# Kernel optimization log

Measured on AMD Instinct MI355X. Metric: run time of the kernel, lower is better.

The kernel has to match this reference:

```python
import math
import jax, jax.numpy as jnp
import numpy as np
from jax import lax

B, S, T = 16, 1200, 600
D, V, FF = 1024, 1404, 2048
H, DH, PERIOD, WID = 4, 256, 25, 8


def setup_inputs() -> dict:
    key = jax.random.key(0)
    ks = jax.random.split(key, 24)
    w = lambda i, shape: jax.random.normal(ks[i], shape, dtype=jnp.float32) * 0.02
    return {
        "audio_embedding": jax.random.normal(ks[0], (B, S, 768), dtype=jnp.float32),
        "vertice": jax.random.normal(ks[1], (B, T, 3, 468), dtype=jnp.float32),
        "W_af": w(2, (D, 768)), "b_af": w(3, (D,)),
        "sa_Wq": w(4, (D, D)), "sa_bq": w(5, (D,)),
        "sa_Wk": w(6, (D, D)), "sa_bk": w(7, (D,)),
        "sa_Wv": w(8, (D, D)), "sa_bv": w(9, (D,)),
        "sa_Wo": w(10, (D, D)), "sa_bo": w(11, (D,)),
        "ca_Wq": w(12, (D, D)), "ca_bq": w(13, (D,)),
        "ca_Wk": w(14, (D, D)), "ca_bk": w(15, (D,)),
        "ca_Wv": w(16, (D, D)), "ca_bv": w(17, (D,)),
        "ca_Wo": w(18, (D, D)), "ca_bo": w(19, (D,)),
        "ln1_g": jnp.ones((D,), jnp.float32), "ln1_b": jnp.zeros((D,), jnp.float32),
        "ln2_g": jnp.ones((D,), jnp.float32), "ln2_b": jnp.zeros((D,), jnp.float32),
        "ln3_g": jnp.ones((D,), jnp.float32), "ln3_b": jnp.zeros((D,), jnp.float32),
        "W_ff1": w(20, (FF, D)), "b_ff1": jnp.zeros((FF,), jnp.float32),
        "W_ff2": w(21, (D, FF)), "b_ff2": jnp.zeros((D,), jnp.float32),
        "W_vm": w(22, (D, V)), "b_vm": jnp.zeros((D,), jnp.float32),
        "W_vr": w(23, (V, D)), "b_vr": jnp.zeros((V,), jnp.float32),
    }


def _pe_table():
    # PeriodicPositionalEncoding: sin/cos table of length `period`, tiled over time
    pos = np.arange(PERIOD, dtype=np.float32)[:, None]
    div = np.exp(np.arange(0, D, 2, dtype=np.float32) * (-math.log(10000.0) / D))
    pe = np.zeros((PERIOD, D), dtype=np.float32)
    pe[:, 0::2] = np.sin(pos * div)
    pe[:, 1::2] = np.cos(pos * div)
    return jnp.asarray(pe)


def _slopes():
    start = 2.0 ** (-2.0 ** (-(math.log2(H) - 3.0)))
    return jnp.asarray(start * start ** np.arange(H, dtype=np.float32), dtype=jnp.float32)


def _ln(x, g, b):
    m = jnp.mean(x, -1, keepdims=True)
    v = jnp.mean((x - m) ** 2, -1, keepdims=True)
    return (x - m) / jnp.sqrt(v + 1e-5) * g + b


def reference(audio_embedding, vertice, W_af, b_af, sa_Wq, sa_bq, sa_Wk, sa_bk, sa_Wv, sa_bv, sa_Wo, sa_bo, ca_Wq, ca_bq, ca_Wk, ca_bk, ca_Wv, ca_bv, ca_Wo, ca_bo, ln1_g, ln1_b, ln2_g, ln2_b, ln3_g, ln3_b, W_ff1, b_ff1, W_ff2, b_ff2, W_vm, b_vm, W_vr, b_vr):
    # The torch loop reruns the full causal decoder on the growing prefix each frame;
    # because the tgt mask is strictly causal (ALiBi bias depends only on i-j), the
    # math is exactly equivalent to an incremental decode with a self-attn KV cache.
    pe, slopes = _pe_table(), _slopes()
    scale = 1.0 / math.sqrt(DH)
    NEG = -1e9
    hidden = audio_embedding @ W_af.T + b_af              # (B,S,D) audio_feature_map
    mem_k = (hidden @ ca_Wk.T + ca_bk).reshape(B, S, H, DH)
    mem_v = (hidden @ ca_Wv.T + ca_bv).reshape(B, S, H, DH)
    t_idx = jnp.arange(T)
    s_idx = jnp.arange(S)
    emb0 = jnp.broadcast_to(b_vm, (B, D))                 # vertice_map(zeros)
    kc0 = jnp.zeros((T, B, D), jnp.float32)
    vc0 = jnp.zeros((T, B, D), jnp.float32)

    def step(carry, i):
        emb, kc, vc = carry
        x = emb + pe[i % PERIOD]                          # PPE (B,D)
        q = (x @ sa_Wq.T + sa_bq).reshape(B, H, DH)
        kc = kc.at[i].set(x @ sa_Wk.T + sa_bk)
        vc = vc.at[i].set(x @ sa_Wv.T + sa_bv)
        kh = kc.reshape(T, B, H, DH)
        vh = vc.reshape(T, B, H, DH)
        rel = i - t_idx                                   # ALiBi: alibi[i,j] = -floor((i-j)/period)
        bias = slopes[:, None] * (-(jnp.maximum(rel, 0) // PERIOD)).astype(jnp.float32)
        sc = jnp.einsum('bhd,tbhd->bht', q, kh) * scale + bias[None]
        sc = jnp.where((t_idx <= i)[None, None, :], sc, NEG)
        sa = jnp.einsum('bht,tbhd->bhd', jax.nn.softmax(sc, -1), vh).reshape(B, D)
        x = _ln(x + sa @ sa_Wo.T + sa_bo, ln1_g, ln1_b)
        q2 = (x @ ca_Wq.T + ca_bq).reshape(B, H, DH)
        sc2 = jnp.einsum('bhd,bshd->bhs', q2, mem_k) * scale
        allowed = (s_idx >= 2 * i - (WID - 2)) & (s_idx < 2 * i + 2)   # enc_dec_mask window
        sc2 = jnp.where(allowed[None, None, :], sc2, NEG)
        ca = jnp.einsum('bhs,bshd->bhd', jax.nn.softmax(sc2, -1), mem_v).reshape(B, D)
        x = _ln(x + ca @ ca_Wo.T + ca_bo, ln2_g, ln2_b)
        ff = jax.nn.relu(x @ W_ff1.T + b_ff1) @ W_ff2.T + b_ff2
        x = _ln(x + ff, ln3_g, ln3_b)
        out_v = x @ W_vr.T + b_vr                         # vertice_map_r (B,V)
        emb_next = out_v @ W_vm.T + b_vm                  # vertice_map of last output
        return (emb_next, kc, vc), out_v

    _, outs = lax.scan(step, (emb0, kc0, vc0), t_idx)
    vertice_out = jnp.transpose(outs, (1, 0, 2))          # (B,T,V)
    loss = jnp.mean((vertice_out - vertice.reshape(B, T, -1)) ** 2)
    return loss
```

## Files before the change

### kernel.cpp

```cpp
#include <hip/hip_runtime.h>

typedef unsigned short u16;
typedef short s16x8 __attribute__((ext_vector_type(8)));
typedef float f32x4 __attribute__((ext_vector_type(4)));
typedef float f32x2 __attribute__((ext_vector_type(2)));
typedef unsigned u32x2 __attribute__((ext_vector_type(2)));

#define DEV static __device__ __forceinline__

DEV float bf2f(u16 h){ union{unsigned u;float f;} v; v.u=((unsigned)h)<<16; return v.f; }
DEV u16 f2bf(float f){ union{float f;unsigned u;} v; v.f=f; unsigned u=v.u; return (u16)((u + 0x7fffu + ((u>>16)&1u))>>16); }

DEV void st2_dc(u16* p, u16 v){
  unsigned vv = v;
  asm volatile("global_store_short %0, %1, off sc0 sc1" :: "v"(p), "v"(vv) : "memory");
}
DEV void st16_dc(void* p, s16x8 v){
  asm volatile("global_store_dwordx4 %0, %1, off sc0 sc1" :: "v"(p), "v"(v) : "memory");
}
DEV void stf_dc(float* p, float v){
  asm volatile("global_store_dword %0, %1, off sc0 sc1" :: "v"(p), "v"(v) : "memory");
}
DEV u16 ld2_dc(const u16* p){
  unsigned r;
  asm volatile("global_load_ushort %0, %1, off sc0 sc1\n\ts_waitcnt vmcnt(0)" : "=&v"(r) : "v"(p) : "memory");
  return (u16)r;
}
DEV void vmwait0(){ asm volatile("s_waitcnt vmcnt(0)" ::: "memory"); }

DEV void ldf8_dc(const u16* p, s16x8* o){
  asm volatile(
    "global_load_dwordx4 %0, %8, off sc0 sc1\n\t"
    "global_load_dwordx4 %1, %8, off offset:64 sc0 sc1\n\t"
    "global_load_dwordx4 %2, %8, off offset:128 sc0 sc1\n\t"
    "global_load_dwordx4 %3, %8, off offset:192 sc0 sc1\n\t"
    "global_load_dwordx4 %4, %8, off offset:256 sc0 sc1\n\t"
    "global_load_dwordx4 %5, %8, off offset:320 sc0 sc1\n\t"
    "global_load_dwordx4 %6, %8, off offset:384 sc0 sc1\n\t"
    "global_load_dwordx4 %7, %8, off offset:448 sc0 sc1\n\t"
    "s_waitcnt vmcnt(0)"
    : "=&v"(o[0]),"=&v"(o[1]),"=&v"(o[2]),"=&v"(o[3]),
// ... 3 lines not shown
DEV void ldf8r_dc(const u16* p, s16x8* o, const u16* pr, unsigned* rr){
  asm volatile(
    "global_load_dwordx4 %0, %9, off sc0 sc1\n\t"
    "global_load_dwordx4 %1, %9, off offset:64 sc0 sc1\n\t"
    "global_load_dwordx4 %2, %9, off offset:128 sc0 sc1\n\t"
    "global_load_dwordx4 %3, %9, off offset:192 sc0 sc1\n\t"
    "global_load_dwordx4 %4, %9, off offset:256 sc0 sc1\n\t"
    "global_load_dwordx4 %5, %9, off offset:320 sc0 sc1\n\t"
    "global_load_dwordx4 %6, %9, off offset:384 sc0 sc1\n\t"
    "global_load_dwordx4 %7, %9, off offset:448 sc0 sc1\n\t"
    "global_load_ushort %8, %10, off sc0 sc1\n\t"
    "s_waitcnt vmcnt(0)"
    : "=&v"(o[0]),"=&v"(o[1]),"=&v"(o[2]),"=&v"(o[3]),
      "=&v"(o[4]),"=&v"(o[5]),"=&v"(o[6]),"=&v"(o[7]),"=&v"(*rr)
    : "v"(p), "v"(pr) : "memory");
}
DEV void ldf8rs_dc(const u16* p, s16x8* o, const u16* pr, unsigned* rr, const float* ps, f32x2* ss){
  asm volatile(
    "global_load_dwordx4 %0, %10, off sc0 sc1\n\t"
    "global_load_dwordx4 %1, %10, off offset:64 sc0 sc1\n\t"
    "global_load_dwordx4 %2, %10, off offset:128 sc0 sc1\n\t"
    "global_load_dwordx4 %3, %10, off offset:192 sc0 sc1\n\t"
    "global_load_dwordx4 %4, %10, off offset:256 sc0 sc1\n\t"
    "global_load_dwordx4 %5, %10, off offset:320 sc0 sc1\n\t"
    "global_load_dwordx4 %6, %10, off offset:384 sc0 sc1\n\t"
    "global_load_dwordx4 %7, %10, off offset:448 sc0 sc1\n\t"
    "global_load_ushort %8, %11, off sc0 sc1\n\t"
    "global_load_dwordx2 %9, %12, off sc0 sc1\n\t"
    "s_waitcnt vmcnt(0)"
    : "=&v"(o[0]),"=&v"(o[1]),"=&v"(o[2]),"=&v"(o[3]),
      "=&v"(o[4]),"=&v"(o[5]),"=&v"(o[6]),"=&v"(o[7]),"=&v"(*rr),"=&v"(*ss)
    : "v"(p), "v"(pr), "v"(ps) : "memory");
}
DEV void ldf16rs_dc(const u16* p, s16x8* o, const u16* pr, unsigned* rr, const float* ps, f32x2* ss){
  asm volatile(
    "global_load_dwordx4 %0, %18, off sc0 sc1\n\t"
    "global_load_dwordx4 %1, %18, off offset:64 sc0 sc1\n\t"
    "global_load_dwordx4 %2, %18, off offset:128 sc0 sc1\n\t"
    "global_load_dwordx4 %3, %18, off offset:192 sc0 sc1\n\t"
    "global_load_dwordx4 %4, %18, off offset:256 sc0 sc1\n\t"
    "global_load_dwordx4 %5, %18, off offset:320 sc0 sc1\n\t"
    "global_load_dwordx4 %6, %18, off offset:384 sc0 sc1\n\t"
    "global_load_dwordx4 %7, %18, off offset:448 sc0 sc1\n\t"
    "global_load_dwordx4 %8, %18, off offset:2048 sc0 sc1\n\t"
    "global_load_dwordx4 %9, %18, off offset:2112 sc0 sc1\n\t"
    "global_load_dwordx4 %10, %18, off offset:2176 sc0 sc1\n\t"
    "global_load_dwordx4 %11, %18, off offset:2240 sc0 sc1\n\t"
// ... 4 lines not shown
    "global_load_ushort %16, %19, off sc0 sc1\n\t"
    "global_load_dwordx2 %17, %20, off sc0 sc1\n\t"
    "s_waitcnt vmcnt(0)"
    : "=&v"(o[0]),"=&v"(o[1]),"=&v"(o[2]),"=&v"(o[3]),
      "=&v"(o[4]),"=&v"(o[5]),"=&v"(o[6]),"=&v"(o[7]),
      "=&v"(o[8]),"=&v"(o[9]),"=&v"(o[10]),"=&v"(o[11]),
      "=&v"(o[12]),"=&v"(o[13]),"=&v"(o[14]),"=&v"(o[15]),
      "=&v"(*rr),"=&v"(*ss)
    : "v"(p), "v"(pr), "v"(ps) : "memory");
}

constexpr size_t SZ_DD = (size_t)1024*1024*2;
constexpr size_t OFF_WQ2=0;
constexpr size_t OFF_WK2=OFF_WQ2+SZ_DD;
constexpr size_t OFF_WV2=OFF_WK2+SZ_DD;
constexpr size_t OFF_WO=OFF_WV2+SZ_DD;
constexpr size_t OFF_CAWQ=OFF_WO+SZ_DD;
constexpr size_t OFF_CAWO=OFF_CAWQ+SZ_DD;
constexpr size_t OFF_FF1=OFF_CAWO+SZ_DD;
constexpr size_t OFF_FF2=OFF_FF1+(size_t)2048*1024*2;
constexpr size_t OFF_MB =OFF_FF2+(size_t)2048*1024*2;
constexpr size_t OFF_WVR=OFF_MB+SZ_DD;
constexpr size_t OFF_WKP=OFF_WVR+(size_t)1404*1024*2;
constexpr size_t OFF_WVP=OFF_WKP+(size_t)1024*768*2;
constexpr size_t OFF_WAFT=OFF_WVP+(size_t)1024*768*2;
constexpr size_t OFF_WVRT=OFF_WAFT+(size_t)768*1024*2;
constexpr size_t OFF_PE  =OFF_WVRT+(size_t)1024*1408*2;
constexpr size_t OFF_BKP =OFF_PE+25*1024*4;
constexpr size_t OFF_BVP =OFF_BKP+4096;
constexpr size_t OFF_BCOMB=OFF_BVP+4096;
constexpr size_t OFF_MEMK=OFF_BCOMB+4096;
constexpr size_t OFF_MEMV=OFF_MEMK+(size_t)16*1200*1024*2;
constexpr size_t OFF_KC  =OFF_MEMV+(size_t)16*1200*1024*2;
constexpr size_t OFF_VC  =OFF_KC+(size_t)600*16*1024*2;
constexpr size_t OFF_U3S =OFF_VC+(size_t)600*16*1024*2;
constexpr size_t OFF_ST3 =OFF_U3S+(size_t)600*16*1024*2;
constexpr size_t OFF_XB  =OFF_ST3+600*32*4;
constexpr size_t OFF_QB  =OFF_XB+32768;
constexpr size_t OFF_SC  =OFF_QB+32768;
constexpr size_t OFF_SA  =OFF_SC+(size_t)16*4*608*4;
constexpr size_t OFF_U1  =OFF_SA+32768;
constexpr size_t OFF_ST1 =OFF_U1+32768;
constexpr size_t OFF_Q2  =OFF_ST1+256;
constexpr size_t OFF_CA  =OFF_Q2+32768;
constexpr size_t OFF_U2  =OFF_CA+32768;
constexpr size_t OFF_ST2 =OFF_U2+32768;
constexpr size_t OFF_HH  =OFF_ST2+256;
constexpr size_t OFF_LOSS=OFF_HH+65536;
constexpr size_t OFF_BAR =OFF_LOSS+256;
constexpr size_t OFF_MBT =OFF_BAR+32768;
constexpr size_t OFF_AT  =OFF_MBT+SZ_DD;
constexpr size_t WS_NEED =OFF_AT+(size_t)3*25*1024*4;

DEV float gemm_frag(const s16x8* a, const u16* slot, float* FB){
  int tid=threadIdx.x, wv=tid>>6, ln=tid&63;
  int r=ln&15, kq=ln>>4;
  int k0=wv*256 + kq*8;
  int sw=(r&7)<<3;
  const u16* bp = slot + r*1024;
  f32x4 acc={0.f,0.f,0.f,0.f};
// ... 34 lines not shown
    s16x8 o;
    #pragma unroll
    for(int e=0;e<8;e++){ int k=32*j+e; float f=(bf2f((u16)a[j][e])-m)*rs*gg[k]+bb[k]; o[e]=(short)f2bf(f); }
    a[j]=o;
  }
}

DEV void copy_slot(const u16* src, int rstride, u16* dst){
  int row=threadIdx.x>>4, k0=(threadIdx.x&15)<<6;
  int sw=(row&7)<<3;
  const u16* s = src + (size_t)row*rstride + k0;
  u16* d = dst + row*1024;
  #pragma unroll
  for(int c=0;c<64;c+=8)
    *(s16x8*)(d + (((k0+c))^sw)) = *(const s16x8*)(s+c);
}

DEV void gbar_pc(char* barb, unsigned& epoch, int wg, int pf, int pc){
  vmwait0();
  __syncthreads();
  unsigned target = epoch + 1u;
  if (threadIdx.x == 0)
    __hip_atomic_store((unsigned*)(barb + (wg<<7)), target, __ATOMIC_RELAXED, __HIP_MEMORY_SCOPE_AGENT);
  if ((int)threadIdx.x < pc){
    unsigned* s = (unsigned*)(barb + ((pf + threadIdx.x)<<7));
    while (__hip_atomic_load(s, __ATOMIC_RELAXED, __HIP_MEMORY_SCOPE_AGENT) < target)
      __builtin_amdgcn_s_sleep(1);
  }
  __syncthreads();
  epoch++;
// ... 33 lines not shown
  for(int p=0;p<4;p++){ int jj=j0+lr+p*8, rr=r0+lj;
    if (jj<C && rr<ldd) dst[(size_t)jj*ldd+rr] = f2bf(TL[lj][lr+p*8]); }
}

__global__ void __launch_bounds__(256) k_trb(const u16* src, u16* dst){
  __shared__ u16 T[32][33];
  int bi=blockIdx.x>>5, bj=blockIdx.x&31;
  int li=threadIdx.x>>5, lj=threadIdx.x&31;
  #pragma unroll
  for(int p=0;p<4;p++) T[li+p*8][lj] = src[(size_t)(bi*32+li+p*8)*1024 + bj*32+lj];
  __syncthreads();
  #pragma unroll
  for(int p=0;p<4;p++) dst[(size_t)(bj*32+li+p*8)*1024 + bi*32+lj] = T[lj][li+p*8];
}

DEV float gemm_tile16g(const u16* SLu, int lds_stride, const u16* W, int Kext, int wstride, int colbase, float* FB){
  int tid=threadIdx.x, wv=tid>>6, ln=tid&63;
  int r=ln&15, kq=ln>>4;
  int kpw=Kext>>2, k0=wv*kpw;
  const u16* ap = SLu + r*lds_stride + k0 + kq*8;
  const u16* bp = W + (size_t)(colbase+r)*wstride + k0 + kq*8;
  f32x4 acc={0.f,0.f,0.f,0.f};
  for(int k=0;k<kpw;k+=32)
    acc = __builtin_amdgcn_mfma_f32_16x16x32_bf16(*(const s16x8*)(ap+k), *(const s16x8*)(bp+k), acc, 0,0,0);
  #pragma unroll
  for(int j=0;j<4;j++) FB[wv*256 + (kq*4+j)*16 + r] = acc[j];
  __syncthreads();
  int row=tid>>4, col=tid&15;
  float s=(FB[row*16+col]+FB[256+row*16+col])+(FB[512+row*16+col]+FB[768+row*16+col]);
  __syncthreads();
  return s;
}

__global__ void __launch_bounds__(256) k_gemm_pre(const float* A, int lda, int Kreal, int Kpad,
                                                  const u16* Bw, u16* out, int ldo, int Ntiles){
  __shared__ u16 SL[16*1416];
  __shared__ float FB[1024];
  int bx=blockIdx.x; int mt=bx/Ntiles, nt=bx%Ntiles;
  int tid=threadIdx.x;
  int cpt = Kpad>>4;
  { int row=tid>>4, c0=(tid&15)*cpt;
    const float* s=A + (size_t)(mt*16+row)*lda;
    u16* d=SL + row*(Kpad+8);
    for(int c=0;c<cpt;c++){ int k=c0+c; d[k] = (k<Kreal)? f2bf(s[k]) : (u16)0; }
    __syncthreads();
  }
  float v = gemm_tile16g(SL, Kpad+8, Bw, Kpad, Kpad, nt*16, FB);
  int row=tid>>4, col=tid&15;
  out[(size_t)(mt*16+row)*ldo + nt*16+col] = f2bf(v);
}

__global__ void __launch_bounds__(256) k_bvec(const float* caWk, const float* ca_bk, const float* b_af,
                                              const float* caWv, const float* ca_bv,
                                              const float* Wvm, const float* b_vr, const float* b_vm,
                                              float* bkp, float* bvp, float* bcomb){
  __shared__ float VB[1408];
  int seg=blockIdx.x>>2, ch=blockIdx.x&3; int o=ch*256+threadIdx.x;
  const float* vec = (seg==2)? b_vr : b_af; int K = (seg==2)?1404:1024;
  for(int k=threadIdx.x;k<K;k+=256) VB[k]=vec[k];
  __syncthreads();
  const float* Arow = (seg==0)? caWk+(size_t)o*1024 : (seg==1)? caWv+(size_t)o*1024 : Wvm+(size_t)o*1404;
  float s=0.f;
  for(int k=0;k<K;k++) s += Arow[k]*VB[k];
  if(seg==0) bkp[o]=s+ca_bk[o]; else if(seg==1) bvp[o]=s+ca_bv[o]; else bcomb[o]=s+b_vm[o];
}

__global__ void __launch_bounds__(256) k_afold(const float* pe, const float* bcomb,
                                               const float* Wq, const float* Wk, const float* Wv,
                                               const float* bq, const float* bk, const float* bv,
                                               float* at){
  __shared__ float XV[1024];
  int bx=blockIdx.x; int mat=bx/100; int rem=bx%100; int ip=rem>>2; int ch=rem&3;
  const float* W = (mat==0)?Wq:(mat==1)?Wk:Wv;
  const float* bias = (mat==0)?bq:(mat==1)?bk:bv;
  for(int o=threadIdx.x;o<1024;o+=256) XV[o]=bcomb[o]+pe[ip*1024+o];
  __syncthreads();
  int c = ch*256+threadIdx.x;
  const float* wr = W + (size_t)c*1024;
  float acc=0.f;
// ... 13 lines not shown
  if (mat==3){
    u16 hv = f2bf(XV[c]);
    for(int r=0;r<16;r++) xb[r*1024+c]=hv;
  } else {
    const float* W = (mat==0)?Wq:(mat==1)?Wk:Wv;
    const float* bias = (mat==0)?bq:(mat==1)?bk:bv;
    const float* wr = W + (size_t)c*1024;
    float acc=0.f;
    for(int o=0;o<1024;o++) acc += XV[o]*wr[o];
    u16 hv = f2bf(acc + bias[c]);
    u16* dst = (mat==0)? qb : (mat==1)? kc : vc;
    for(int r=0;r<16;r++) dst[r*1024+c]=hv;
  }
}

__global__ void __launch_bounds__(256) k_mem(const float* audio, const u16* wkp, const u16* wvp,
                                             const float* bkp, const float* bvp, u16* mt8, u16* memv){
  __shared__ u16 SL[16*776];
  int bx=blockIdx.x; int mt=bx>>3, cbk=bx&7;
  int tid=threadIdx.x, wv=tid>>6, ln=tid&63;
  { int row=tid>>4, c0=(tid&15)*48;
    const float* s = audio + (size_t)(mt*16+row)*768 + c0;
    u16* d = SL + row*776 + c0;
    #pragma unroll
    for(int c=0;c<48;c+=8){ s16x8 o;
      #pragma unroll
      for(int j=0;j<8;j++) o[j]=(short)f2bf(s[c+j]);
      *(s16x8*)(d+c)=o; }
    __syncthreads();
  }
  int r=ln&15, kq=ln>>4;
  const u16* ap = SL + r*776 + kq*8;
  for(int rep=0;rep<2;rep++){
    int colb = cbk*128 + wv*32 + rep*16;
    for(int mat=0;mat<2;mat++){
      const u16* W = mat? wvp : wkp;
      const u16* bp = W + (size_t)(colb+r)*768 + kq*8;
      f32x4 acc={0.f,0.f,0.f,0.f};
      for(int k=0;k<768;k+=32)
        acc = __builtin_amdgcn_mfma_f32_16x16x32_bf16(*(const s16x8*)(ap+k), *(const s16x8*)(bp+k), acc, 0,0,0);
      const float* bias = mat? bvp:bkp;
      int o = colb + r;
      float bo = bias[o];
      #pragma unroll
      for(int j=0;j<4;j++){ int row_=kq*4+j;
        int g = mt*16+row_;
        float val = acc[j] + bo;
        if (mat){
          memv[(size_t)g*1024 + o] = f2bf(val);
        } else {
          int bb=g/1200, ss=g-bb*1200;
          mt8[(((size_t)(bb*4 + (o>>8))*32 + ((o&255)>>3))*1200 + ss)*8 + (o&7)] = f2bf(val);
        }
      }
    }
  }
}

struct LoopArgs {
  const float *sa_bo,*ca_bq,*ca_bo,*b_ff1,*b_ff2;
  const float *g1,*be1,*g2,*be2,*g3,*be3;
  char* ws;
};

__global__ void __launch_bounds__(256,1) k_loop(LoopArgs A){
  __shared__ u16 WL[3*16*1024];
  __shared__ float FB[1024];
  __shared__ float PL[608];
  __shared__ float RB[640];
  __shared__ float STm[16], STr[16];

  char* ws = A.ws;
  const u16* wq2  =(const u16*)(ws+OFF_WQ2);
  const u16* wk2  =(const u16*)(ws+OFF_WK2);
  const u16* wv2  =(const u16*)(ws+OFF_WV2);
  const u16* wo   =(const u16*)(ws+OFF_WO);
  const u16* cawq =(const u16*)(ws+OFF_CAWQ);
  const u16* cawo =(const u16*)(ws+OFF_CAWO);
  const u16* ff1  =(const u16*)(ws+OFF_FF1);
  const u16* ff2  =(const u16*)(ws+OFF_FF2);
  const u16* mb   =(const u16*)(ws+OFF_MB);
  const float* pe =(const float*)(ws+OFF_PE);
  const float* bcomb=(const float*)(ws+OFF_BCOMB);
  const float* at =(const float*)(ws+OFF_AT);
  const u16* mt8  =(const u16*)(ws+OFF_MEMK);
  const u16* memv =(const u16*)(ws+OFF_MEMV);
  u16* kc =(u16*)(ws+OFF_KC);
  u16* vc =(u16*)(ws+OFF_VC);
  u16* u3s=(u16*)(ws+OFF_U3S);
  float* st3=(float*)(ws+OFF_ST3);
  u16* xb =(u16*)(ws+OFF_XB);
  u16* qb =(u16*)(ws+OFF_QB);
  u16* sab=(u16*)(ws+OFF_SA);
  u16* u1 =(u16*)(ws+OFF_U1);
  float* st1=(float*)(ws+OFF_ST1);
  u16* q2b=(u16*)(ws+OFF_Q2);
  u16* cab=(u16*)(ws+OFF_CA);
  u16* u2 =(u16*)(ws+OFF_U2);
  float* st2=(float*)(ws+OFF_ST2);
  u16* hh =(u16*)(ws+OFF_HH);
  char* barb=(char*)(ws+OFF_BAR);

  unsigned epoch = 0;
  int wg = blockIdx.x, tid = threadIdx.x;
  int row = tid>>4, lo = tid&15;
  int wv = tid>>6, ln = tid&63;
  int fr = ln&15, kq = ln>>4;
  int k0 = wv*256 + kq*8;
  int grp = wg>>6, ct = (wg&63)<<4;

  {
    u16* s0d = WL;          u16* s1d = WL+16384;  u16* s2d = WL+32768;
    if (grp==0){
      copy_slot(wq2 +(size_t)ct*1024,1024,s0d);
      copy_slot(cawq+(size_t)ct*1024,1024,s1d);
      copy_slot(ff1 +(size_t)ct*1024,1024,s2d);
    } else if (grp==1){
      copy_slot(wk2 +(size_t)ct*1024,1024,s0d);
      copy_slot(cawo+(size_t)ct*1024,1024,s1d);
      copy_slot(ff1 +((size_t)(1024+ct))*1024,1024,s2d);
    } else if (grp==2){
      copy_slot(wv2 +(size_t)ct*1024,1024,s0d);
      copy_slot(ff2 +(size_t)ct*2048,2048,s1d);
      copy_slot(ff2 +(size_t)ct*2048+1024,2048,s2d);
    } else {
      copy_slot(mb  +(size_t)ct*1024,1024,s0d);
      copy_slot(wo  +(size_t)ct*1024,1024,s1d);
    }
    __syncthreads();
  }
  const u16* SLOT0 = WL;
  const u16* SLOT1 = WL+16384;
  const u16* SLOT2 = WL+32768;

// ... 60 lines not shown
        for(int j=0;j<8;j++) o8[j]=(short)f2bf(acc[j]*rl);
        st16_dc(sab + b*1024 + h*256 + d_oct*8, o8);
      }
    }
    gbar_pc(barb, epoch, wg, 0, (wg>=192)?64:0);

    if (wg>=192){
      s16x8 f[8]; unsigned er;
      ldf8r_dc(sab + fr*1024 + k0, f, xb + row*1024 + ct + lo, &er);
      float v = gemm_frag(f,SLOT1,FB);
      int o = ct+lo;
      st2_dc(u1 + row*1024 + o, f2bf(bf2f((u16)er) + v + A.sa_bo[o]));
    }
    gbar_pc(barb, epoch, wg, 192, (wg<64)?64:0);

    if (wg<64){
      s16x8 f[8];
      ldf8_dc(u1 + fr*1024 + k0, f);
      ln_frags(f, A.g1, A.be1, k0, fr, RB, STm, STr);
      float v = gemm_frag(f,SLOT1,FB);
      int o=ct+lo;
      st2_dc(q2b + row*1024+o, f2bf(v + A.ca_bq[o]));
      if (wg==0 && tid<16){ stf_dc(st1+tid*2, STm[tid]); stf_dc(st1+tid*2+1, STr[tid]); }
    }
    gbar_pc(barb, epoch, wg, 0, (wg<64)?64:0);

    if (wg<64){
      int b=wg>>2, h=wg&3;
      RB[tid] = bf2f(ld2_dc(q2b + b*1024 + h*256 + tid));
      __syncthreads();
      int s0 = 2*i-6; if(s0<0)s0=0;
      int s1 = 2*i+2; if(s1>1200)s1=1200;
      int ns = s1-s0;
      int si=tid>>5, dl=tid&31;
      float p=0.f;
      if (si<ns){
        const u16* MT = mt8 + (((size_t)(b*4+h)*32 + dl)*1200 + (s0+si))*8;
        s16x8 m8 = *(const s16x8*)MT;
        #pragma unroll
        for(int j=0;j<8;j++) p += RB[dl*8+j]*bf2f((u16)m8[j]);
      }
      #pragma unroll
      for(int o2=16;o2>0;o2>>=1) p += __shfl_xor(p,o2);
      if (dl==0 && si<ns) RB[512+si] = p*0.0625f;
      __syncthreads();
      float mx=-1e30f;
      for(int qd=0;qd<ns;qd++) mx=fmaxf(mx,RB[512+qd]);
      float l=0.f, acc2=0.f;
      for(int qd=0;qd<ns;qd++){
        float e=__expf(RB[512+qd]-mx); l+=e;
        acc2 += e*bf2f(memv[(size_t)(b*1200+s0+qd)*1024 + h*256 + tid]);
      }
      st2_dc(cab + b*1024+h*256+tid, f2bf(acc2/l));
    }
    gbar_pc(barb, epoch, wg, 0, (wg>=64&&wg<128)?64:0);

    if (wg>=64 && wg<128){
      s16x8 f[8]; unsigned ur; f32x2 sv;
      ldf8rs_dc(cab + fr*1024 + k0, f, u1 + row*1024 + ct + lo, &ur, st1 + row*2, &sv);
      float v = gemm_frag(f,SLOT1,FB);
      int o=ct+lo;
      float x1 = (bf2f((u16)ur)-sv[0])*sv[1]*A.g1[o] + A.be1[o];
      st2_dc(u2+row*1024+o, f2bf(x1 + v + A.ca_bo[o]));
    }
    gbar_pc(barb, epoch, wg, 64, (wg<128)?64:0);

    if (wg<128){
      s16x8 f[8];
      ldf8_dc(u2 + fr*1024 + k0, f);
      ln_frags(f, A.g2, A.be2, k0, fr, RB, STm, STr);
      float v = gemm_frag(f,SLOT2,FB);
      int o=(wg<<4)+lo;
      st2_dc(hh+row*2048+o, f2bf(fmaxf(v + A.b_ff1[o], 0.f)));
      if (wg==0 && tid<16){ stf_dc(st2+tid*2,STm[tid]); stf_dc(st2+tid*2+1,STr[tid]); }
    }
    gbar_pc(barb, epoch, wg, 0, (wg>=128&&wg<192)?128:0);

    if (wg>=128 && wg<192){
      s16x8 f[16]; unsigned ur; f32x2 sv;
      ldf16rs_dc(hh + fr*2048 + k0, f, u2 + row*1024 + ct + lo, &ur, st2 + row*2, &sv);
// ... 98 lines not shown
  const float* caWq =(const float*)d_in[12]; const float* ca_bq=(const float*)d_in[13];
  const float* caWk =(const float*)d_in[14]; const float* ca_bk=(const float*)d_in[15];
  const float* caWv =(const float*)d_in[16]; const float* ca_bv=(const float*)d_in[17];
  const float* caWo =(const float*)d_in[18]; const float* ca_bo=(const float*)d_in[19];
  const float* g1=(const float*)d_in[20]; const float* be1=(const float*)d_in[21];
  const float* g2=(const float*)d_in[22]; const float* be2=(const float*)d_in[23];
  const float* g3=(const float*)d_in[24]; const float* be3=(const float*)d_in[25];
  const float* Wff1=(const float*)d_in[26]; const float* b_ff1=(const float*)d_in[27];
  const float* Wff2=(const float*)d_in[28]; const float* b_ff2=(const float*)d_in[29];
  const float* Wvm=(const float*)d_in[30];  const float* b_vm=(const float*)d_in[31];
  const float* Wvr=(const float*)d_in[32];  const float* b_vr=(const float*)d_in[33];

  k_init<<<1,256,0,stream>>>((float*)(ws+OFF_PE), (float*)(ws+OFF_LOSS), (unsigned*)(ws+OFF_BAR));

  k_f2bf<<<512,256,0,stream>>>(caWq,(u16*)(ws+OFF_CAWQ),1048576);
  k_f2bf<<<512,256,0,stream>>>(caWo,(u16*)(ws+OFF_CAWO),1048576);
  k_f2bf<<<512,256,0,stream>>>(saWo,(u16*)(ws+OFF_WO),1048576);
  k_f2bf<<<1024,256,0,stream>>>(Wff1,(u16*)(ws+OFF_FF1),2097152);
  k_f2bf<<<1024,256,0,stream>>>(Wff2,(u16*)(ws+OFF_FF2),2097152);
  k_f2bf<<<702,256,0,stream>>>(Wvr,(u16*)(ws+OFF_WVR),1437696);

  k_tr<<<24*32,256,0,stream>>>(W_af, 1024, 768, (u16*)(ws+OFF_WAFT), 1024);
  k_tr<<<32*44,256,0,stream>>>(Wvr, 1404, 1024, (u16*)(ws+OFF_WVRT), 1408);

  k_gemm_pre<<<64*48,256,0,stream>>>(caWk, 1024, 1024, 1024, (const u16*)(ws+OFF_WAFT), (u16*)(ws+OFF_WKP), 768, 48);
  k_gemm_pre<<<64*48,256,0,stream>>>(caWv, 1024, 1024, 1024, (const u16*)(ws+OFF_WAFT), (u16*)(ws+OFF_WVP), 768, 48);
  k_gemm_pre<<<64*64,256,0,stream>>>(Wvm, 1404, 1404, 1408, (const u16*)(ws+OFF_WVRT), (u16*)(ws+OFF_MB), 1024, 64);

  k_trb<<<1024,256,0,stream>>>((const u16*)(ws+OFF_MB), (u16*)(ws+OFF_MBT));
  k_gemm_pre<<<64*64,256,0,stream>>>(saWq, 1024, 1024, 1024, (const u16*)(ws+OFF_MBT), (u16*)(ws+OFF_WQ2), 1024, 64);
  k_gemm_pre<<<64*64,256,0,stream>>>(saWk, 1024, 1024, 1024, (const u16*)(ws+OFF_MBT), (u16*)(ws+OFF_WK2), 1024, 64);
  k_gemm_pre<<<64*64,256,0,stream>>>(saWv, 1024, 1024, 1024, (const u16*)(ws+OFF_MBT), (u16*)(ws+OFF_WV2), 1024, 64);

  k_bvec<<<12,256,0,stream>>>(caWk, ca_bk, b_af, caWv, ca_bv, Wvm, b_vr, b_vm,
                              (float*)(ws+OFF_BKP),(float*)(ws+OFF_BVP),(float*)(ws+OFF_BCOMB));

  k_afold<<<300,256,0,stream>>>((const float*)(ws+OFF_PE), (const float*)(ws+OFF_BCOMB),
                                saWq, saWk, saWv, sa_bq, sa_bk, sa_bv, (float*)(ws+OFF_AT));

  k_qkv0<<<16,256,0,stream>>>(b_vm, (const float*)(ws+OFF_PE), saWq, saWk, saWv, sa_bq, sa_bk, sa_bv,
                              (u16*)(ws+OFF_QB), (u16*)(ws+OFF_KC), (u16*)(ws+OFF_VC), (u16*)(ws+OFF_XB));

  k_mem<<<9600,256,0,stream>>>(audio, (const u16*)(ws+OFF_WKP),(const u16*)(ws+OFF_WVP),
                               (const float*)(ws+OFF_BKP),(const float*)(ws+OFF_BVP),
                               (u16*)(ws+OFF_MEMK),(u16*)(ws+OFF_MEMV));

  LoopArgs la{ sa_bo, ca_bq, ca_bo, b_ff1, b_ff2,
               g1, be1, g2, be2, g3, be3, ws };
  k_loop<<<256,256,0,stream>>>(la);

  k_loss<<<825,256,0,stream>>>((const u16*)(ws+OFF_U3S),(const float*)(ws+OFF_ST3),
                               (const u16*)(ws+OFF_WVR), b_vr, g3, be3, vert, (float*)(ws+OFF_LOSS));
  k_fin<<<1,64,0,stream>>>((const float*)(ws+OFF_LOSS), (float*)d_out);
}
```

Measured before the change: 33.53 ms.

## Fold cross-attention output projection into per-head value memory with rolling ring buffer

```diff
diff --git a/kernel.cpp b/kernel.cpp
--- a/kernel.cpp
+++ b/kernel.cpp
@@ -15,6 +15,9 @@
   unsigned vv = v;
   asm volatile("global_store_short %0, %1, off sc0 sc1" :: "v"(p), "v"(vv) : "memory");
 }
+DEV void st8_dc(u16* p, u32x2 v){
+  asm volatile("global_store_dwordx2 %0, %1, off sc0 sc1" :: "v"(p), "v"(v) : "memory");
+}
 DEV void st16_dc(void* p, s16x8 v){
   asm volatile("global_store_dwordx4 %0, %1, off sc0 sc1" :: "v"(p), "v"(v) : "memory");
 }
@@ -25,6 +28,16 @@
   unsigned r;
   asm volatile("global_load_ushort %0, %1, off sc0 sc1\n\ts_waitcnt vmcnt(0)" : "=&v"(r) : "v"(p) : "memory");
   return (u16)r;
+}
+DEV void ld8x2_dc(const u16* p1, const u16* p2, u32x2* a, u32x2* b){
+  asm volatile(
+    "global_load_dwordx2 %0, %2, off sc0 sc1\n\t"
+    "global_load_dwordx2 %1, %3, off sc0 sc1\n\t"
+    "s_waitcnt vmcnt(0)"
+    : "=&v"(*a), "=&v"(*b) : "v"(p1), "v"(p2) : "memory");
+}
+DEV void ld8_nw2(const u16* p, u32x2* d){
+  asm volatile("global_load_dwordx2 %0, %1, off sc0 sc1" : "=&v"(*d) : "v"(p) : "memory");
 }
 DEV void vmwait0(){ asm volatile("s_waitcnt vmcnt(0)" ::: "memory"); }
 
@@ -58,23 +71,6 @@
     : "=&v"(o[0]),"=&v"(o[1]),"=&v"(o[2]),"=&v"(o[3]),
       "=&v"(o[4]),"=&v"(o[5]),"=&v"(o[6]),"=&v"(o[7]),"=&v"(*rr)
     : "v"(p), "v"(pr) : "memory");
-}
-DEV void ldf8rs_dc(const u16* p, s16x8* o, const u16* pr, unsigned* rr, const float* ps, f32x2* ss){
-  asm volatile(
-    "global_load_dwordx4 %0, %10, off sc0 sc1\n\t"
-    "global_load_dwordx4 %1, %10, off offset:64 sc0 sc1\n\t"
-    "global_load_dwordx4 %2, %10, off offset:128 sc0 sc1\n\t"
-    "global_load_dwordx4 %3, %10, off offset:192 sc0 sc1\n\t"
-    "global_load_dwordx4 %4, %10, off offset:256 sc0 sc1\n\t"
-    "global_load_dwordx4 %5, %10, off offset:320 sc0 sc1\n\t"
-    "global_load_dwordx4 %6, %10, off offset:384 sc0 sc1\n\t"
-    "global_load_dwordx4 %7, %10, off offset:448 sc0 sc1\n\t"
-    "global_load_ushort %8, %11, off sc0 sc1\n\t"
-    "global_load_dwordx2 %9, %12, off sc0 sc1\n\t"
-    "s_waitcnt vmcnt(0)"
-    : "=&v"(o[0]),"=&v"(o[1]),"=&v"(o[2]),"=&v"(o[3]),
-      "=&v"(o[4]),"=&v"(o[5]),"=&v"(o[6]),"=&v"(o[7]),"=&v"(*rr),"=&v"(*ss)
-    : "v"(p), "v"(pr), "v"(ps) : "memory");
 }
 DEV void ldf16rs_dc(const u16* p, s16x8* o, const u16* pr, unsigned* rr, const float* ps, f32x2* ss){
   asm volatile(
@@ -109,36 +105,35 @@
 constexpr size_t OFF_WQ2=0;
 constexpr size_t OFF_WK2=OFF_WQ2+SZ_DD;
 constexpr size_t OFF_WV2=OFF_WK2+SZ_DD;
-constexpr size_t OFF_WO=OFF_WV2+SZ_DD;
+constexpr size_t OFF_WO =OFF_WV2+SZ_DD;
 constexpr size_t OFF_CAWQ=OFF_WO+SZ_DD;
-constexpr size_t OFF_CAWO=OFF_CAWQ+SZ_DD;
-constexpr size_t OFF_FF1=OFF_CAWO+SZ_DD;
+constexpr size_t OFF_FF1=OFF_CAWQ+SZ_DD;
 constexpr size_t OFF_FF2=OFF_FF1+(size_t)2048*1024*2;
 constexpr size_t OFF_MB =OFF_FF2+(size_t)2048*1024*2;
 constexpr size_t OFF_WVR=OFF_MB+SZ_DD;
 constexpr size_t OFF_WKP=OFF_WVR+(size_t)1404*1024*2;
 constexpr size_t OFF_WVP=OFF_WKP+(size_t)1024*768*2;
-constexpr size_t OFF_WAFT=OFF_WVP+(size_t)1024*768*2;
+constexpr size_t OFF_WVPT=OFF_WVP+(size_t)1024*768*2;
+constexpr size_t OFF_WAFT=OFF_WVPT+(size_t)768*1024*2;
 constexpr size_t OFF_WVRT=OFF_WAFT+(size_t)768*1024*2;
-constexpr size_t OFF_PE  =OFF_WVRT+(size_t)1024*1408*2;
-constexpr size_t OFF_BKP =OFF_PE+25*1024*4;
+constexpr size_t OFF_PCAT=OFF_WVRT+(size_t)1024*1408*2;
+constexpr size_t OFF_QCAT=OFF_PCAT+(size_t)4096*768*2;
+constexpr size_t OFF_PE  =OFF_QCAT+16384;
+constexpr size_t OFF_BKP =OFF_PE+102400;
 constexpr size_t OFF_BVP =OFF_BKP+4096;
 constexpr size_t OFF_BCOMB=OFF_BVP+4096;
 constexpr size_t OFF_MEMK=OFF_BCOMB+4096;
-constexpr size_t OFF_MEMV=OFF_MEMK+(size_t)16*1200*1024*2;
-constexpr size_t OFF_KC  =OFF_MEMV+(size_t)16*1200*1024*2;
+constexpr size_t OFF_MVOR=OFF_MEMK+(size_t)16*1200*1024*2;
+constexpr size_t OFF_KC  =OFF_MVOR+(size_t)32*16*4096*2;
 constexpr size_t OFF_VC  =OFF_KC+(size_t)600*16*1024*2;
 constexpr size_t OFF_U3S =OFF_VC+(size_t)600*16*1024*2;
 constexpr size_t OFF_ST3 =OFF_U3S+(size_t)600*16*1024*2;
-constexpr size_t OFF_XB  =OFF_ST3+600*32*4;
+constexpr size_t OFF_XB  =OFF_ST3+76800;
 constexpr size_t OFF_QB  =OFF_XB+32768;
-constexpr size_t OFF_SC  =OFF_QB+32768;
-constexpr size_t OFF_SA  =OFF_SC+(size_t)16*4*608*4;
+constexpr size_t OFF_SA  =OFF_QB+32768;
 constexpr size_t OFF_U1  =OFF_SA+32768;
-constexpr size_t OFF_ST1 =OFF_U1+32768;
-constexpr size_t OFF_Q2  =OFF_ST1+256;
-constexpr size_t OFF_CA  =OFF_Q2+32768;
-constexpr size_t OFF_U2  =OFF_CA+32768;
+constexpr size_t OFF_Q2  =OFF_U1+32768;
+constexpr size_t OFF_U2  =OFF_Q2+32768;
 constexpr size_t OFF_ST2 =OFF_U2+32768;
 constexpr size_t OFF_HH  =OFF_ST2+256;
 constexpr size_t OFF_LOSS=OFF_HH+65536;
@@ -203,6 +198,24 @@
   #pragma unroll
   for(int c=0;c<64;c+=8)
     *(s16x8*)(d + (((k0+c))^sw)) = *(const s16x8*)(s+c);
+}
+
+DEV float gemm_tile16g(const u16* SLu, int lds_stride, const u16* W, int Kext, int wstride, int colbase, float* FB){
+  int tid=threadIdx.x, wv=tid>>6, ln=tid&63;
+  int r=ln&15, kq=ln>>4;
+  int kpw=Kext>>2, k0=wv*kpw;
+  const u16* ap = SLu + r*lds_stride + k0 + kq*8;
+  const u16* bp = W + (size_t)(colbase+r)*wstride + k0 + kq*8;
+  f32x4 acc={0.f,0.f,0.f,0.f};
+  for(int k=0;k<kpw;k+=32)
+    acc = __builtin_amdgcn_mfma_f32_16x16x32_bf16(*(const s16x8*)(ap+k), *(const s16x8*)(bp+k), acc, 0,0,0);
+  #pragma unroll
+  for(int j=0;j<4;j++) FB[wv*256 + (kq*4+j)*16 + r] = acc[j];
+  __syncthreads();
+  int row=tid>>4, col=tid&15;
+  float s=(FB[row*16+col]+FB[256+row*16+col])+(FB[512+row*16+col]+FB[768+row*16+col]);
+  __syncthreads();
+  return s;
 }
 
 DEV void gbar_pc(char* barb, unsigned& epoch, int wg, int pf, int pc){
@@ -266,26 +279,21 @@
   for(int p=0;p<4;p++) dst[(size_t)(bj*32+li+p*8)*1024 + bi*32+lj] = T[lj][li+p*8];
 }
 
-DEV float gemm_tile16g(const u16* SLu, int lds_stride, const u16* W, int Kext, int wstride, int colbase, float* FB){
-  int tid=threadIdx.x, wv=tid>>6, ln=tid&63;
-  int r=ln&15, kq=ln>>4;
-  int kpw=Kext>>2, k0=wv*kpw;
-  const u16* ap = SLu + r*lds_stride + k0 + kq*8;
-  const u16* bp = W + (size_t)(colbase+r)*wstride + k0 + kq*8;
-  f32x4 acc={0.f,0.f,0.f,0.f};
-  for(int k=0;k<kpw;k+=32)
-    acc = __builtin_amdgcn_mfma_f32_16x16x32_bf16(*(const s16x8*)(ap+k), *(const s16x8*)(bp+k), acc, 0,0,0);
-  #pragma unroll
-  for(int j=0;j<4;j++) FB[wv*256 + (kq*4+j)*16 + r] = acc[j];
-  __syncthreads();
-  int row=tid>>4, col=tid&15;
-  float s=(FB[row*16+col]+FB[256+row*16+col])+(FB[512+row*16+col]+FB[768+row*16+col]);
-  __syncthreads();
-  return s;
+__global__ void __launch_bounds__(256) k_trbg(const u16* src, int R, int C, u16* dst){
+  __shared__ u16 T[32][33];
+  int cb=C>>5;
+  int br=blockIdx.x/cb, bc=blockIdx.x%cb;
+  int r0=br*32, c0=bc*32;
+  int lr=threadIdx.x>>5, lc=threadIdx.x&31;
+  #pragma unroll
+  for(int p=0;p<4;p++) T[lr+p*8][lc] = src[(size_t)(r0+lr+p*8)*C + c0+lc];
+  __syncthreads();
+  #pragma unroll
+  for(int p=0;p<4;p++) dst[(size_t)(c0+lr+p*8)*R + r0+lc] = T[lc][lr+p*8];
 }
 
 __global__ void __launch_bounds__(256) k_gemm_pre(const float* A, int lda, int Kreal, int Kpad,
-                                                  const u16* Bw, u16* out, int ldo, int Ntiles){
+                                                  const u16* Bw, int wstride, u16* out, int ldo, int Ntiles){
   __shared__ u16 SL[16*1416];
   __shared__ float FB[1024];
   int bx=blockIdx.x; int mt=bx/Ntiles, nt=bx%Ntiles;
@@ -297,7 +305,7 @@
     for(int c=0;c<cpt;c++){ int k=c0+c; d[k] = (k<Kreal)? f2bf(s[k]) : (u16)0; }
     __syncthreads();
   }
-  float v = gemm_tile16g(SL, Kpad+8, Bw, Kpad, Kpad, nt*16, FB);
+  float v = gemm_tile16g(SL, Kpad+8, Bw, Kpad, wstride, nt*16, FB);
   int row=tid>>4, col=tid&15;
   out[(size_t)(mt*16+row)*ldo + nt*16+col] = f2bf(v);
 }
@@ -315,6 +323,18 @@
   float s=0.f;
   for(int k=0;k<K;k++) s += Arow[k]*VB[k];
   if(seg==0) bkp[o]=s+ca_bk[o]; else if(seg==1) bvp[o]=s+ca_bv[o]; else bcomb[o]=s+b_vm[o];
+}
+
+__global__ void __launch_bounds__(256) k_qcat(const float* caWo, const float* bvp, float* qcat){
+  __shared__ float BV[256];
+  int h=blockIdx.x>>2, ch=blockIdx.x&3;
+  for(int d=threadIdx.x; d<256; d+=256) BV[d]=bvp[h*256+d];
+  __syncthreads();
+  int o = ch*256+threadIdx.x;
+  const float* wr = caWo + (size_t)o*1024 + h*256;
+  float s=0.f;
+  for(int d=0;d<256;d++) s += BV[d]*wr[d];
+  qcat[h*1024+o]=s;
 }
 
 __global__ void __launch_bounds__(256) k_afold(const float* pe, const float* bcomb,
@@ -358,8 +378,7 @@
   }
 }
 
-__global__ void __launch_bounds__(256) k_mem(const float* audio, const u16* wkp, const u16* wvp,
-                                             const float* bkp, const float* bvp, u16* mt8, u16* memv){
+__global__ void __launch_bounds__(256) k_mem(const float* audio, const u16* wkp, const float* bkp, u16* mt8){
   __shared__ u16 SL[16*776];
   int bx=blockIdx.x; int mt=bx>>3, cbk=bx&7;
   int tid=threadIdx.x, wv=tid>>6, ln=tid&63;
@@ -377,33 +396,48 @@
   const u16* ap = SL + r*776 + kq*8;
   for(int rep=0;rep<2;rep++){
     int colb = cbk*128 + wv*32 + rep*16;
-    for(int mat=0;mat<2;mat++){
-      const u16* W = mat? wvp : wkp;
-      const u16* bp = W + (size_t)(colb+r)*768 + kq*8;
-      f32x4 acc={0.f,0.f,0.f,0.f};
-      for(int k=0;k<768;k+=32)
-        acc = __builtin_amdgcn_mfma_f32_16x16x32_bf16(*(const s16x8*)(ap+k), *(const s16x8*)(bp+k), acc, 0,0,0);
-      const float* bias = mat? bvp:bkp;
-      int o = colb + r;
-      float bo = bias[o];
-      #pragma unroll
-      for(int j=0;j<4;j++){ int row_=kq*4+j;
-        int g = mt*16+row_;
-        float val = acc[j] + bo;
-        if (mat){
-          memv[(size_t)g*1024 + o] = f2bf(val);
-        } else {
-          int bb=g/1200, ss=g-bb*1200;
-          mt8[(((size_t)(bb*4 + (o>>8))*32 + ((o&255)>>3))*1200 + ss)*8 + (o&7)] = f2bf(val);
-        }
-      }
-    }
+    const u16* bp = wkp + (size_t)(colb+r)*768 + kq*8;
+    f32x4 acc={0.f,0.f,0.f,0.f};
+    for(int k=0;k<768;k+=32)
+      acc = __builtin_amdgcn_mfma_f32_16x16x32_bf16(*(const s16x8*)(ap+k), *(const s16x8*)(bp+k), acc, 0,0,0);
+    int o = colb + r;
+    float bo = bkp[o];
+    #pragma unroll
+    for(int j=0;j<4;j++){ int row_=kq*4+j;
+      int g = mt*16+row_;
+      int bb=g/1200, ss=g-bb*1200;
+      mt8[(((size_t)(bb*4 + (o>>8))*32 + ((o&255)>>3))*1200 + ss)*8 + (o&7)] = f2bf(acc[j]+bo);
+    }
+  }
+}
+
+__global__ void __launch_bounds__(256) k_mvo(const float* audio, const u16* pcat, const float* qcat, u16* ring){
+  __shared__ u16 SL[16*776];
+  __shared__ float FB[1024];
+  int s = blockIdx.x>>5, cbk = blockIdx.x&31;
+  int tid=threadIdx.x;
+  { int row=tid>>4, c0=(tid&15)*48;
+    const float* src = audio + ((size_t)row*1200 + s)*768 + c0;
+    u16* d = SL + row*776 + c0;
+    #pragma unroll
+    for(int c=0;c<48;c+=8){ s16x8 o;
+      #pragma unroll
+      for(int j=0;j<8;j++) o[j]=(short)f2bf(src[c+j]);
+      *(s16x8*)(d+c)=o; }
+    __syncthreads();
+  }
+  for(int t=0;t<8;t++){
+    int colbase = cbk*128 + t*16;
+    float v = gemm_tile16g(SL, 776, pcat, 768, 768, colbase, FB);
+    int b=tid>>4, col=colbase+(tid&15);
+    ring[((size_t)s*16 + b)*4096 + col] = f2bf(v + qcat[col]);
   }
 }
 
 struct LoopArgs {
   const float *sa_bo,*ca_bq,*ca_bo,*b_ff1,*b_ff2;
   const float *g1,*be1,*g2,*be2,*g3,*be3;
+  const float *audio;
   char* ws;
 };
 
@@ -413,6 +447,7 @@
   __shared__ float PL[608];
   __shared__ float RB[640];
   __shared__ float STm[16], STr[16];
+  __shared__ u16 AB[16*776];
 
   char* ws = A.ws;
   const u16* wq2  =(const u16*)(ws+OFF_WQ2);
@@ -420,15 +455,16 @@
   const u16* wv2  =(const u16*)(ws+OFF_WV2);
   const u16* wo   =(const u16*)(ws+OFF_WO);
   const u16* cawq =(const u16*)(ws+OFF_CAWQ);
-  const u16* cawo =(const u16*)(ws+OFF_CAWO);
   const u16* ff1  =(const u16*)(ws+OFF_FF1);
   const u16* ff2  =(const u16*)(ws+OFF_FF2);
   const u16* mb   =(const u16*)(ws+OFF_MB);
+  const u16* pcat =(const u16*)(ws+OFF_PCAT);
+  const float* qcat=(const float*)(ws+OFF_QCAT);
   const float* pe =(const float*)(ws+OFF_PE);
   const float* bcomb=(const float*)(ws+OFF_BCOMB);
   const float* at =(const float*)(ws+OFF_AT);
   const u16* mt8  =(const u16*)(ws+OFF_MEMK);
-  const u16* memv =(const u16*)(ws+OFF_MEMV);
+  u16* ring=(u16*)(ws+OFF_MVOR);
   u16* kc =(u16*)(ws+OFF_KC);
   u16* vc =(u16*)(ws+OFF_VC);
   u16* u3s=(u16*)(ws+OFF_U3S);
@@ -437,9 +473,7 @@
   u16* qb =(u16*)(ws+OFF_QB);
   u16* sab=(u16*)(ws+OFF_SA);
   u16* u1 =(u16*)(ws+OFF_U1);
-  float* st1=(float*)(ws+OFF_ST1);
   u16* q2b=(u16*)(ws+OFF_Q2);
-  u16* cab=(u16*)(ws+OFF_CA);
   u16* u2 =(u16*)(ws+OFF_U2);
   float* st2=(float*)(ws+OFF_ST2);
   u16* hh =(u16*)(ws+OFF_HH);
@@ -461,7 +495,6 @@
       copy_slot(ff1 +(size_t)ct*1024,1024,s2d);
     } else if (grp==1){
       copy_slot(wk2 +(size_t)ct*1024,1024,s0d);
-      copy_slot(cawo+(size_t)ct*1024,1024,s1d);
       copy_slot(ff1 +((size_t)(1024+ct))*1024,1024,s2d);
     } else if (grp==2){
       copy_slot(wv2 +(size_t)ct*1024,1024,s0d);
@@ -552,6 +585,27 @@
     }
     gbar_pc(barb, epoch, wg, 192, (wg<64)?64:0);
 
+    if (wg>=128 && wg<192 && i<596){
+      int p=wg-128, sl=p>>5, cb=p&31;
+      int s=2*i+8+sl;
+      { int rr=tid>>4, c0=(tid&15)*48;
+        const float* src = A.audio + ((size_t)rr*1200 + s)*768 + c0;
+        u16* d = AB + rr*776 + c0;
+        #pragma unroll
+        for(int c=0;c<48;c+=8){ s16x8 o;
+          #pragma unroll
+          for(int j=0;j<8;j++) o[j]=(short)f2bf(src[c+j]);
+          *(s16x8*)(d+c)=o; }
+        __syncthreads();
+      }
+      for(int t=0;t<8;t++){
+        int colbase = cb*128 + t*16;
+        float v = gemm_tile16g(AB, 776, pcat, 768, 768, colbase, FB);
+        int b=tid>>4, col=colbase+(tid&15);
+        st2_dc(ring + ((size_t)(s&31)*16 + b)*4096 + col, f2bf(v + qcat[col]));
+      }
+    }
+
     if (wg<64){
       s16x8 f[8];
       ldf8_dc(u1 + fr*1024 + k0, f);
@@ -559,49 +613,90 @@
       float v = gemm_frag(f,SLOT1,FB);
       int o=ct+lo;
       st2_dc(q2b + row*1024+o, f2bf(v + A.ca_bq[o]));
-      if (wg==0 && tid<16){ stf_dc(st1+tid*2, STm[tid]); stf_dc(st1+tid*2+1, STr[tid]); }
-    }
-    gbar_pc(barb, epoch, wg, 0, (wg<64)?64:0);
-
-    if (wg<64){
-      int b=wg>>2, h=wg&3;
-      RB[tid] = bf2f(ld2_dc(q2b + b*1024 + h*256 + tid));
+    }
+    gbar_pc(barb, epoch, wg, 0, (wg<16)?64:0);
+
+    if (wg < 16){
+      int b = wg;
+      int c0 = tid*4;
+      u32x2 qq, uu;
+      ld8x2_dc(q2b + b*1024 + c0, u1 + b*1024 + c0, &qq, &uu);
+      FB[c0+0]=bf2f((u16)(qq[0]&0xffffu)); FB[c0+1]=bf2f((u16)(qq[0]>>16));
+      FB[c0+2]=bf2f((u16)(qq[1]&0xffffu)); FB[c0+3]=bf2f((u16)(qq[1]>>16));
+      float e0=bf2f((u16)(uu[0]&0xffffu)), e1=bf2f((u16)(uu[0]>>16));
+      float e2=bf2f((u16)(uu[1]&0xffffu)), e3=bf2f((u16)(uu[1]>>16));
+      float s4=(e0+e1)+(e2+e3);
+      float q4=(e0*e0+e1*e1)+(e2*e2+e3*e3);
+      #pragma unroll
+      for(int off=32;off>0;off>>=1){ s4+=__shfl_down(s4,off); q4+=__shfl_down(q4,off); }
+      if (ln==0){ RB[608+wv]=s4; RB[616+wv]=q4; }
       __syncthreads();
-      int s0 = 2*i-6; if(s0<0)s0=0;
-      int s1 = 2*i+2; if(s1>1200)s1=1200;
-      int ns = s1-s0;
-      int si=tid>>5, dl=tid&31;
-      float p=0.f;
-      if (si<ns){
-        const u16* MT = mt8 + (((size_t)(b*4+h)*32 + dl)*1200 + (s0+si))*8;
-        s16x8 m8 = *(const s16x8*)MT;
+      float S=(RB[608]+RB[609])+(RB[610]+RB[611]);
+      float Q=(RB[616]+RB[617])+(RB[618]+RB[619]);
+      float m=S*(1.f/1024.f);
+      float rs=rsqrtf(Q*(1.f/1024.f)-m*m+1e-5f);
+      int s0w = 2*i-6; if(s0w<0)s0w=0;
+      int s1w = 2*i+2; if(s1w>1200)s1w=1200;
+      int ns = s1w-s0w;
+      int oc = tid&31, hs0 = tid>>5;
+      #pragma unroll
+      for(int rr=0;rr<4;rr++){
+        int hs = hs0 + 8*rr; int h = hs>>3, si = hs&7;
+        float part=0.f;
+        if (si<ns){
+          s16x8 k8 = *(const s16x8*)(mt8 + (((size_t)(b*4+h)*32 + oc)*1200 + (s0w+si))*8);
+          #pragma unroll
+          for(int e=0;e<8;e++) part += FB[h*256 + oc*8 + e]*bf2f((u16)k8[e]);
+        }
         #pragma unroll
-        for(int j=0;j<8;j++) p += RB[dl*8+j]*bf2f((u16)m8[j]);
-      }
-      #pragma unroll
-      for(int o2=16;o2>0;o2>>=1) p += __shfl_xor(p,o2);
-      if (dl==0 && si<ns) RB[512+si] = p*0.0625f;
+        for(int off=16;off>0;off>>=1) part += __shfl_xor(part,off);
+        if (oc==0) RB[hs] = part*0.0625f;
+      }
       __syncthreads();
-      float mx=-1e30f;
-      for(int qd=0;qd<ns;qd++) mx=fmaxf(mx,RB[512+qd]);
-      float l=0.f, acc2=0.f;
-      for(int qd=0;qd<ns;qd++){
-        float e=__expf(RB[512+qd]-mx); l+=e;
-        acc2 += e*bf2f(memv[(size_t)(b*1200+s0+qd)*1024 + h*256 + tid]);
-      }
-      st2_dc(cab + b*1024+h*256+tid, f2bf(acc2/l));
-    }
-    gbar_pc(barb, epoch, wg, 0, (wg>=64&&wg<128)?64:0);
-
-    if (wg>=64 && wg<128){
-      s16x8 f[8]; unsigned ur; f32x2 sv;
-      ldf8rs_dc(cab + fr*1024 + k0, f, u1 + row*1024 + ct + lo, &ur, st1 + row*2, &sv);
-      float v = gemm_frag(f,SLOT1,FB);
-      int o=ct+lo;
-      float x1 = (bf2f((u16)ur)-sv[0])*sv[1]*A.g1[o] + A.be1[o];
-      st2_dc(u2+row*1024+o, f2bf(x1 + v + A.ca_bo[o]));
-    }
-    gbar_pc(barb, epoch, wg, 64, (wg<128)?64:0);
+      float mh[4], lh[4];
+      #pragma unroll
+      for(int h=0;h<4;h++){
+        float mx=-1e30f;
+        for(int si=0;si<ns;si++) mx=fmaxf(mx,RB[h*8+si]);
+        float l=0.f;
+        for(int si=0;si<ns;si++) l+=__expf(RB[h*8+si]-mx);
+        mh[h]=mx; lh[h]=1.f/l;
+      }
+      float a4[4]={0.f,0.f,0.f,0.f};
+      #pragma unroll
+      for(int hp=0; hp<2; hp++){
+        u32x2 buf[16];
+        #pragma unroll
+        for(int h2=0;h2<2;h2++){
+          int h=hp*2+h2;
+          #pragma unroll
+          for(int si=0;si<8;si++){
+            int ss = (si<ns)? si : 0;
+            ld8_nw2(ring + ((size_t)(((s0w+ss)&31))*16 + b)*4096 + h*1024 + c0, &buf[h2*8+si]);
+          }
+        }
+        vmwait0();
+        #pragma unroll
+        for(int h2=0;h2<2;h2++){
+          int h=hp*2+h2;
+          for(int si=0;si<ns;si++){
+            float w = __expf(RB[h*8+si]-mh[h])*lh[h];
+            u32x2 vv = buf[h2*8+si];
+            a4[0]+=w*bf2f((u16)(vv[0]&0xffffu)); a4[1]+=w*bf2f((u16)(vv[0]>>16));
+            a4[2]+=w*bf2f((u16)(vv[1]&0xffffu)); a4[3]+=w*bf2f((u16)(vv[1]>>16));
+          }
+        }
+      }
+      float o0=(e0-m)*rs*A.g1[c0]  +A.be1[c0]  +a4[0]+A.ca_bo[c0];
+      float o1=(e1-m)*rs*A.g1[c0+1]+A.be1[c0+1]+a4[1]+A.ca_bo[c0+1];
+      float o2=(e2-m)*rs*A.g1[c0+2]+A.be1[c0+2]+a4[2]+A.ca_bo[c0+2];
+      float o3=(e3-m)*rs*A.g1[c0+3]+A.be1[c0+3]+a4[3]+A.ca_bo[c0+3];
+      u32x2 ov;
+      ov[0] = (unsigned)f2bf(o0) | ((unsigned)f2bf(o1)<<16);
+      ov[1] = (unsigned)f2bf(o2) | ((unsigned)f2bf(o3)<<16);
+      st8_dc(u2 + b*1024 + c0, ov);
+    }
+    gbar_pc(barb, epoch, wg, 0, (wg<128)?16:0);
 
     if (wg<128){
       s16x8 f[8];
@@ -730,7 +825,6 @@
   k_init<<<1,256,0,stream>>>((float*)(ws+OFF_PE), (float*)(ws+OFF_LOSS), (unsigned*)(ws+OFF_BAR));
 
   k_f2bf<<<512,256,0,stream>>>(caWq,(u16*)(ws+OFF_CAWQ),1048576);
-  k_f2bf<<<512,256,0,stream>>>(caWo,(u16*)(ws+OFF_CAWO),1048576);
   k_f2bf<<<512,256,0,stream>>>(saWo,(u16*)(ws+OFF_WO),1048576);
   k_f2bf<<<1024,256,0,stream>>>(Wff1,(u16*)(ws+OFF_FF1),2097152);
   k_f2bf<<<1024,256,0,stream>>>(Wff2,(u16*)(ws+OFF_FF2),2097152);
@@ -739,17 +833,25 @@
   k_tr<<<24*32,256,0,stream>>>(W_af, 1024, 768, (u16*)(ws+OFF_WAFT), 1024);
   k_tr<<<32*44,256,0,stream>>>(Wvr, 1404, 1024, (u16*)(ws+OFF_WVRT), 1408);
 
-  k_gemm_pre<<<64*48,256,0,stream>>>(caWk, 1024, 1024, 1024, (const u16*)(ws+OFF_WAFT), (u16*)(ws+OFF_WKP), 768, 48);
-  k_gemm_pre<<<64*48,256,0,stream>>>(caWv, 1024, 1024, 1024, (const u16*)(ws+OFF_WAFT), (u16*)(ws+OFF_WVP), 768, 48);
-  k_gemm_pre<<<64*64,256,0,stream>>>(Wvm, 1404, 1404, 1408, (const u16*)(ws+OFF_WVRT), (u16*)(ws+OFF_MB), 1024, 64);
+  k_gemm_pre<<<64*48,256,0,stream>>>(caWk, 1024, 1024, 1024, (const u16*)(ws+OFF_WAFT), 1024, (u16*)(ws+OFF_WKP), 768, 48);
+  k_gemm_pre<<<64*48,256,0,stream>>>(caWv, 1024, 1024, 1024, (const u16*)(ws+OFF_WAFT), 1024, (u16*)(ws+OFF_WVP), 768, 48);
+  k_gemm_pre<<<64*64,256,0,stream>>>(Wvm, 1404, 1404, 1408, (const u16*)(ws+OFF_WVRT), 1408, (u16*)(ws+OFF_MB), 1024, 64);
 
   k_trb<<<1024,256,0,stream>>>((const u16*)(ws+OFF_MB), (u16*)(ws+OFF_MBT));
-  k_gemm_pre<<<64*64,256,0,stream>>>(saWq, 1024, 1024, 1024, (const u16*)(ws+OFF_MBT), (u16*)(ws+OFF_WQ2), 1024, 64);
-  k_gemm_pre<<<64*64,256,0,stream>>>(saWk, 1024, 1024, 1024, (const u16*)(ws+OFF_MBT), (u16*)(ws+OFF_WK2), 1024, 64);
-  k_gemm_pre<<<64*64,256,0,stream>>>(saWv, 1024, 1024, 1024, (const u16*)(ws+OFF_MBT), (u16*)(ws+OFF_WV2), 1024, 64);
+  k_gemm_pre<<<64*64,256,0,stream>>>(saWq, 1024, 1024, 1024, (const u16*)(ws+OFF_MBT), 1024, (u16*)(ws+OFF_WQ2), 1024, 64);
+  k_gemm_pre<<<64*64,256,0,stream>>>(saWk, 1024, 1024, 1024, (const u16*)(ws+OFF_MBT), 1024, (u16*)(ws+OFF_WK2), 1024, 64);
+  k_gemm_pre<<<64*64,256,0,stream>>>(saWv, 1024, 1024, 1024, (const u16*)(ws+OFF_MBT), 1024, (u16*)(ws+OFF_WV2), 1024, 64);
+
+  k_trbg<<<32*24,256,0,stream>>>((const u16*)(ws+OFF_WVP), 1024, 768, (u16*)(ws+OFF_WVPT));
+  for (int h=0;h<4;h++){
+    k_gemm_pre<<<64*48,256,0,stream>>>(caWo + h*256, 1024, 256, 256,
+                                       (const u16*)(ws+OFF_WVPT) + h*256, 1024,
+                                       (u16*)(ws+OFF_PCAT) + (size_t)h*1024*768, 768, 48);
+  }
 
   k_bvec<<<12,256,0,stream>>>(caWk, ca_bk, b_af, caWv, ca_bv, Wvm, b_vr, b_vm,
                               (float*)(ws+OFF_BKP),(float*)(ws+OFF_BVP),(float*)(ws+OFF_BCOMB));
+  k_qcat<<<16,256,0,stream>>>(caWo, (const float*)(ws+OFF_BVP), (float*)(ws+OFF_QCAT));
 
   k_afold<<<300,256,0,stream>>>((const float*)(ws+OFF_PE), (const float*)(ws+OFF_BCOMB),
                                 saWq, saWk, saWv, sa_bq, sa_bk, sa_bv, (float*)(ws+OFF_AT));
@@ -757,12 +859,11 @@
   k_qkv0<<<16,256,0,stream>>>(b_vm, (const float*)(ws+OFF_PE), saWq, saWk, saWv, sa_bq, sa_bk, sa_bv,
                               (u16*)(ws+OFF_QB), (u16*)(ws+OFF_KC), (u16*)(ws+OFF_VC), (u16*)(ws+OFF_XB));
 
-  k_mem<<<9600,256,0,stream>>>(audio, (const u16*)(ws+OFF_WKP),(const u16*)(ws+OFF_WVP),
-                               (const float*)(ws+OFF_BKP),(const float*)(ws+OFF_BVP),
-                               (u16*)(ws+OFF_MEMK),(u16*)(ws+OFF_MEMV));
+  k_mem<<<9600,256,0,stream>>>(audio, (const u16*)(ws+OFF_WKP), (const float*)(ws+OFF_BKP), (u16*)(ws+OFF_MEMK));
+  k_mvo<<<256,256,0,stream>>>(audio, (const u16*)(ws+OFF_PCAT), (const float*)(ws+OFF_QCAT), (u16*)(ws+OFF_MVOR));
 
   LoopArgs la{ sa_bo, ca_bq, ca_bo, b_ff1, b_ff2,
-               g1, be1, g2, be2, g3, be3, ws };
+               g1, be1, g2, be2, g3, be3, audio, ws };
   k_loop<<<256,256,0,stream>>>(la);
 
   k_loss<<<825,256,0,stream>>>((const u16*)(ws+OFF_U3S),(const float*)(ws+OFF_ST3),
```

Result: slower. 37.56 ms (+12.0%).
